# Kernel optimization log

Measured on AMD Instinct MI355X. Metric: run time of the kernel, lower is better.

The kernel has to match this reference:

```python
import jax, jax.numpy as jnp
import numpy as np

B, N, D_IN, D_HID, D_EDGE = 4, 256, 256, 256, 64


def setup_inputs() -> dict:
    key = jax.random.key(0)
    ks = jax.random.split(key, 8)
    s_in = 1.0 / np.sqrt(D_IN)
    s_h2 = 1.0 / np.sqrt(2 * D_HID)
    s_h = 1.0 / np.sqrt(D_HID)
    return {
        "x": jax.random.normal(ks[0], (B, N, D_IN), jnp.float32),
        "W_in": jax.random.uniform(ks[1], (D_HID, D_IN), jnp.float32, -s_in, s_in),
        "b_in": jax.random.uniform(ks[2], (D_HID,), jnp.float32, -s_in, s_in),
        "W1": jax.random.uniform(ks[3], (D_HID, 2 * D_HID), jnp.float32, -s_h2, s_h2),
        "b1": jax.random.uniform(ks[4], (D_HID,), jnp.float32, -s_h2, s_h2),
        "W2": jax.random.uniform(ks[5], (D_EDGE, D_HID), jnp.float32, -s_h, s_h),
        "b2": jax.random.uniform(ks[6], (D_EDGE,), jnp.float32, -s_h, s_h),
    }


def reference(x, W_in, b_in, W1, b1, W2, b2):
    # in_proj: [B,N,d_in] -> [B,N,h]
    h = jnp.einsum("bnd,hd->bnh", x, W_in) + b_in
    # cat([h_i, h_j]) @ W1 == h_i @ Wa + h_j @ Wb with W1 = [Wa | Wb].
    # Precompute the two N x h projections, then broadcast-add over the pair grid
    # instead of materializing the [B,N,N,2h] concat (same math, fused form).
    Wa, Wb = W1[:, :D_HID], W1[:, D_HID:]
    pa = jnp.einsum("bnh,gh->bng", h, Wa)  # [B,N,h]
    pb = jnp.einsum("bnh,gh->bng", h, Wb)  # [B,N,h]
    z = pa[:, :, None, :] + pb[:, None, :, :] + b1  # [B,N,N,h]
    z = z * jax.nn.sigmoid(z)  # Swish
    return jnp.einsum("bijh,eh->bije", z, W2) + b2  # [B,N,N,d_edge]
```

## Files before the change

kernel.cpp:

```cpp
#include <hip/hip_runtime.h>

#define DIN 256
#define DHID 256
#define DEDGE 64
#define GS 68
#define W2_PAD 264

typedef float f32x4 __attribute__((ext_vector_type(4)));
typedef short s16x8 __attribute__((ext_vector_type(8)));
typedef unsigned int u32x4 __attribute__((ext_vector_type(4)));

__device__ __forceinline__ unsigned short f2bf(float f) {
    unsigned int u = __builtin_bit_cast(unsigned int, f);
    u += 0x7fffu + ((u >> 16) & 1u);
    return (unsigned short)(u >> 16);
}
__device__ __forceinline__ unsigned int pk_bf16(float a, float b) {
    return (unsigned int)f2bf(a) | ((unsigned int)f2bf(b) << 16);
}

__global__ __launch_bounds__(256) void k_xh(
    const float* __restrict__ x, const float* __restrict__ Win,
    float* __restrict__ hp)
{
    __shared__ float as[64 * GS];
    __shared__ float ws[64 * GS];
    const int m0 = blockIdx.x << 6, n0 = blockIdx.y << 6, k0 = blockIdx.z << 6;
    const int tid = threadIdx.x;
    const int rr = tid >> 4;
    const int kk = (tid & 15) << 2;

#pragma unroll
    for (int it = 0; it < 4; ++it) {
        const int row = rr + (it << 4);
        *reinterpret_cast<f32x4*>(&as[row * GS + kk]) =
            *reinterpret_cast<const f32x4*>(&x[(m0 + row) * DIN + k0 + kk]);
        *reinterpret_cast<f32x4*>(&ws[row * GS + kk]) =
            *reinterpret_cast<const f32x4*>(&Win[(n0 + row) * DIN + k0 + kk]);
    }
    __syncthreads();

    const int tx = tid & 15, ty = tid >> 4;
    float acc[4][4] = {};
    for (int k = 0; k < 64; k += 4) {
        f32x4 av[4], wv[4];
#pragma unroll
        for (int r = 0; r < 4; ++r)
            av[r] = *reinterpret_cast<const f32x4*>(&as[(ty + (r << 4)) * GS + k]);
#pragma unroll
        for (int c = 0; c < 4; ++c)
            wv[c] = *reinterpret_cast<const f32x4*>(&ws[(tx + (c << 4)) * GS + k]);
#pragma unroll
        for (int r = 0; r < 4; ++r)
#pragma unroll
            for (int c = 0; c < 4; ++c)
                acc[r][c] += av[r][0]*wv[c][0] + av[r][1]*wv[c][1]
                           + av[r][2]*wv[c][2] + av[r][3]*wv[c][3];
    }
    float* dst = hp + ((size_t)blockIdx.z << 18);
#pragma unroll
    for (int r = 0; r < 4; ++r)
#pragma unroll
        for (int c = 0; c < 4; ++c)
            dst[(m0 + ty + (r << 4)) * DHID + n0 + tx + (c << 4)] = acc[r][c];
}

__global__ __launch_bounds__(256) void k_pab(
    const float* __restrict__ hp, const float* __restrict__ W1,
    const float* __restrict__ bin, float* __restrict__ pap, float* __restrict__ pbp)
{
    __shared__ float as[64 * GS];
    __shared__ float ws[64 * GS];
    const int m0 = blockIdx.x << 6;
    const int half = blockIdx.y >> 2;
    const int n0 = (blockIdx.y & 3) << 6;
    const int kc = blockIdx.z;
    const int tid = threadIdx.x;
    const int rr = tid >> 4, kk = (tid & 15) << 2;
    const int tx = tid & 15, ty = tid >> 4;

    float acc[4][4] = {};
    for (int kt = 0; kt < 2; ++kt) {
        const int k0 = (kc << 7) + (kt << 6);
        if (kt) __syncthreads();
#pragma unroll
        for (int it = 0; it < 4; ++it) {
            const int row = rr + (it << 4);
            const int aoff = (m0 + row) * DHID + k0 + kk;
            f32x4 av = *reinterpret_cast<const f32x4*>(&hp[aoff]);
            av += *reinterpret_cast<const f32x4*>(&hp[aoff + (1 << 18)]);
            av += *reinterpret_cast<const f32x4*>(&hp[aoff + (2 << 18)]);
            av += *reinterpret_cast<const f32x4*>(&hp[aoff + (3 << 18)]);
            av += *reinterpret_cast<const f32x4*>(&bin[k0 + kk]);
            *reinterpret_cast<f32x4*>(&as[row * GS + kk]) = av;
            *reinterpret_cast<f32x4*>(&ws[row * GS + kk]) =
                *reinterpret_cast<const f32x4*>(&W1[(n0 + row) * 512 + (half << 8) + k0 + kk]);
        }
        __syncthreads();

        for (int k = 0; k < 64; k += 4) {
            f32x4 av[4], wv[4];
#pragma unroll
            for (int r = 0; r < 4; ++r)
                av[r] = *reinterpret_cast<const f32x4*>(&as[(ty + (r << 4)) * GS + k]);
#pragma unroll
            for (int c = 0; c < 4; ++c)
                wv[c] = *reinterpret_cast<const f32x4*>(&ws[(tx + (c << 4)) * GS + k]);
#pragma unroll
            for (int r = 0; r < 4; ++r)
#pragma unroll
                for (int c = 0; c < 4; ++c)
                    acc[r][c] += av[r][0]*wv[c][0] + av[r][1]*wv[c][1]
                               + av[r][2]*wv[c][2] + av[r][3]*wv[c][3];
        }
    }
    float* dst = (half ? pbp : pap) + ((size_t)kc << 18);
#pragma unroll
    for (int r = 0; r < 4; ++r)
#pragma unroll
        for (int c = 0; c < 4; ++c)
            dst[(m0 + ty + (r << 4)) * DHID + n0 + tx + (c << 4)] = acc[r][c];
}

__global__ __launch_bounds__(256) void k_out(
    const float* __restrict__ pap, const float* __restrict__ pbp,
    const float* __restrict__ b1, const float* __restrict__ W2,
    const float* __restrict__ b2, float* __restrict__ out)
{
    __shared__ unsigned short w2s[DEDGE * W2_PAD];
    __shared__ float pab1[4][DHID];

    const int jb = blockIdx.x, i0 = blockIdx.y << 2, b = blockIdx.z;
    const int tid = threadIdx.x;

    {
        const float b1v = b1[tid];
#pragma unroll
        for (int ii = 0; ii < 4; ++ii) {
            const int off = (((b << 8) + i0 + ii) << 8) + tid;
            pab1[ii][tid] = pap[off] + pap[off + (1 << 18)] + b1v;
        }
    }
#pragma unroll
    for (int it = 0; it < 8; ++it) {
        const int t = tid + (it << 8);
        const int row = t >> 5;
        const int cc = (t & 31) << 3;
        const f32x4 w0 = *reinterpret_cast<const f32x4*>(&W2[row * DHID + cc]);
        const f32x4 w1 = *reinterpret_cast<const f32x4*>(&W2[row * DHID + cc + 4]);
        u32x4 wp;
        wp[0] = pk_bf16(w0[0], w0[1]); wp[1] = pk_bf16(w0[2], w0[3]);
        wp[2] = pk_bf16(w1[0], w1[1]); wp[3] = pk_bf16(w1[2], w1[3]);
        *reinterpret_cast<u32x4*>(&w2s[row * W2_PAD + cc]) = wp;
    }
    __syncthreads();

    const int lane = tid & 63, wave = tid >> 6, quad = lane >> 4, l15 = lane & 15;
    const int j0 = (jb << 6) + (wave << 4);
    const int pboff = (((b << 8) + (j0 + l15)) << 8);
    const float* pbq0 = pbp + pboff;
    const float* pbq1 = pbp + (1 << 18) + pboff;

    f32x4 acc[4][4];
#pragma unroll
    for (int ii = 0; ii < 4; ++ii)
#pragma unroll
        for (int eb = 0; eb < 4; ++eb) acc[ii][eb] = (f32x4){0.f, 0.f, 0.f, 0.f};

    float b2v[4];
#pragma unroll
    for (int eb = 0; eb < 4; ++eb) b2v[eb] = b2[(eb << 4) + l15];

    for (int k0 = 0; k0 < 8; ++k0) {
        const int g = (k0 << 5) + (quad << 3);
        const f32x4 p0 = *reinterpret_cast<const f32x4*>(pbq0 + g)
                       + *reinterpret_cast<const f32x4*>(pbq1 + g);
        const f32x4 p1 = *reinterpret_cast<const f32x4*>(pbq0 + g + 4)
                       + *reinterpret_cast<const f32x4*>(pbq1 + g + 4);

        s16x8 bfrag[4];
#pragma unroll
        for (int eb = 0; eb < 4; ++eb)
            bfrag[eb] = *reinterpret_cast<const s16x8*>(&w2s[((eb << 4) + l15) * W2_PAD + g]);

#pragma unroll
        for (int ii = 0; ii < 4; ++ii) {
            const f32x4 q0 = *reinterpret_cast<const f32x4*>(&pab1[ii][g]);
            const f32x4 q1 = *reinterpret_cast<const f32x4*>(&pab1[ii][g + 4]);
            float s[8];
#pragma unroll
            for (int jj = 0; jj < 4; ++jj) {
                const float z0 = q0[jj] + p0[jj];
                const float z1 = q1[jj] + p1[jj];
                const float e0 = __expf(-z0);
                const float e1 = __expf(-z1);
                s[jj]     = z0 * __builtin_amdgcn_rcpf(1.0f + e0);
                s[4 + jj] = z1 * __builtin_amdgcn_rcpf(1.0f + e1);
            }
            u32x4 ap;
            ap[0] = pk_bf16(s[0], s[1]); ap[1] = pk_bf16(s[2], s[3]);
            ap[2] = pk_bf16(s[4], s[5]); ap[3] = pk_bf16(s[6], s[7]);
            const s16x8 a = __builtin_bit_cast(s16x8, ap);
#pragma unroll
            for (int eb = 0; eb < 4; ++eb)
                acc[ii][eb] = __builtin_amdgcn_mfma_f32_16x16x32_bf16(a, bfrag[eb], acc[ii][eb], 0, 0, 0);
        }
    }

#pragma unroll
    for (int ii = 0; ii < 4; ++ii) {
        const int obase = (((((b << 8) + i0 + ii) << 8) + j0 + (quad << 2)) << 6) + l15;
#pragma unroll
        for (int eb = 0; eb < 4; ++eb) {
#pragma unroll
            for (int r = 0; r < 4; ++r)
                out[obase + (r << 6) + (eb << 4)] = acc[ii][eb][r] + b2v[eb];
        }
    }
}

extern "C" void kernel_launch(void* const* d_in, const int* in_sizes, int n_in,
                              void* d_out, int out_size, void* d_ws, size_t ws_size,
                              hipStream_t stream) {
    const float* x = 0; const float* Win = 0; const float* bin = 0;
    const float* W1 = 0; const float* b1 = 0; const float* W2 = 0; const float* b2 = 0;
    for (int idx = 0; idx < n_in; ++idx) {
        const int s = in_sizes[idx];
        if (s == 262144) x = (const float*)d_in[idx];
        else if (s == 131072) W1 = (const float*)d_in[idx];
        else if (s == 65536) Win = (const float*)d_in[idx];
        else if (s == 16384) W2 = (const float*)d_in[idx];
        else if (s == 64) b2 = (const float*)d_in[idx];
        else if (s == 256) { if (!bin) bin = (const float*)d_in[idx]; else b1 = (const float*)d_in[idx]; }
    }

    float* ws = (float*)d_ws;
    float* hp  = ws;
    float* pap = hp + (4 << 18);
    float* pbp = pap + (2 << 18);

    hipLaunchKernelGGL(k_xh,  dim3(16, 4, 4), dim3(256), 0, stream, x, Win, hp);
    hipLaunchKernelGGL(k_pab, dim3(16, 8, 2), dim3(256), 0, stream, hp, W1, bin, pap, pbp);
    hipLaunchKernelGGL(k_out, dim3(4, 64, 4), dim3(256), 0, stream, pap, pbp, b1, W2, b2, (float*)d_out);
}
```

Before: 130.3 us.

## Fold in_proj into W1, pre-swizzle W2 in LDS, use hardware bf16 packing

Folds the input projection into the first layer by precomputing W1a·Win and W1b·Win plus a combined bias in a small weight-only kernel, so the activation path applies x directly to the combined weights instead of materializing h. W2 is stored in LDS already laid out in MFMA fragment order, so each lane reads its fragment with one indexed load. The software bf16 rounding is replaced with the v_cvt_pk_bf16_f32 instruction, and the large output is written with nontemporal stores. These target the k_out epilogue and conversion overhead and the cost of the first kernel, at the price of a different summation order in the folded weights.

```diff
diff --git a/kernel.cpp b/kernel.cpp
--- a/kernel.cpp
+++ b/kernel.cpp
@@ -4,73 +4,94 @@
 #define DHID 256
 #define DEDGE 64
 #define GS 68
-#define W2_PAD 264
 
 typedef float f32x4 __attribute__((ext_vector_type(4)));
 typedef short s16x8 __attribute__((ext_vector_type(8)));
 typedef unsigned int u32x4 __attribute__((ext_vector_type(4)));
 
-__device__ __forceinline__ unsigned short f2bf(float f) {
-    unsigned int u = __builtin_bit_cast(unsigned int, f);
-    u += 0x7fffu + ((u >> 16) & 1u);
-    return (unsigned short)(u >> 16);
-}
-__device__ __forceinline__ unsigned int pk_bf16(float a, float b) {
-    return (unsigned int)f2bf(a) | ((unsigned int)f2bf(b) << 16);
-}
-
-__global__ __launch_bounds__(256) void k_xh(
-    const float* __restrict__ x, const float* __restrict__ Win,
-    float* __restrict__ hp)
+__device__ __forceinline__ unsigned int cvtpk(float lo, float hi) {
+    unsigned int r;
+    asm("v_cvt_pk_bf16_f32 %0, %1, %2" : "=v"(r) : "v"(lo), "v"(hi));
+    return r;
+}
+
+__global__ __launch_bounds__(256) void k_w(
+    const float* __restrict__ Win, const float* __restrict__ W1,
+    const float* __restrict__ bin, const float* __restrict__ b1,
+    float* __restrict__ CWp, float* __restrict__ cb)
+{
+    const int bid = blockIdx.x;
+    const int tid = threadIdx.x;
+    if (bid == 64) {
+        float acc = b1[tid];
+        const float* wrow = &W1[tid * 512];
+        for (int h = 0; h < 256; h += 4) {
+            const f32x4 wa = *reinterpret_cast<const f32x4*>(&wrow[h]);
+            const f32x4 wb = *reinterpret_cast<const f32x4*>(&wrow[256 + h]);
+            const f32x4 bv = *reinterpret_cast<const f32x4*>(&bin[h]);
+            acc += (wa[0]+wb[0])*bv[0] + (wa[1]+wb[1])*bv[1]
+                 + (wa[2]+wb[2])*bv[2] + (wa[3]+wb[3])*bv[3];
+        }
+        cb[tid] = acc;
+        return;
+    }
+    __shared__ float as[64 * GS];
+    __shared__ float ws2[64 * GS];
+    const int kc = bid >> 5;
+    const int nt = (bid >> 2) & 7;
+    const int dt = bid & 3;
+    const int n0 = nt << 6, d0 = dt << 6;
+    const int na = n0 & 255;
+    const int hb = (n0 >> 8) << 8;
+    const int rr = tid >> 4, kk = (tid & 15) << 2;
+    const int tx = tid & 15, ty = tid >> 4;
+
+    float acc[4][4] = {};
+    for (int kt = 0; kt < 2; ++kt) {
+        const int h0 = (kc << 7) + (kt << 6);
+        if (kt) __syncthreads();
+#pragma unroll
+        for (int it = 0; it < 4; ++it) {
+            const int row = rr + (it << 4);
+            *reinterpret_cast<f32x4*>(&as[row * GS + kk]) =
+                *reinterpret_cast<const f32x4*>(&W1[(na + row) * 512 + hb + h0 + kk]);
+            *reinterpret_cast<f32x4*>(&ws2[row * GS + kk]) =
+                *reinterpret_cast<const f32x4*>(&Win[(h0 + row) * DIN + d0 + kk]);
+        }
+        __syncthreads();
+        for (int k = 0; k < 64; k += 4) {
+            f32x4 av[4];
+#pragma unroll
+            for (int r = 0; r < 4; ++r)
+                av[r] = *reinterpret_cast<const f32x4*>(&as[(ty + (r << 4)) * GS + k]);
+#pragma unroll
+            for (int k2 = 0; k2 < 4; ++k2) {
+                float bcol[4];
+#pragma unroll
+                for (int c = 0; c < 4; ++c)
+                    bcol[c] = ws2[(k + k2) * GS + tx + (c << 4)];
+#pragma unroll
+                for (int r = 0; r < 4; ++r)
+#pragma unroll
+                    for (int c = 0; c < 4; ++c)
+                        acc[r][c] += av[r][k2] * bcol[c];
+            }
+        }
+    }
+    float* dst = CWp + ((size_t)kc << 17);
+#pragma unroll
+    for (int r = 0; r < 4; ++r)
+#pragma unroll
+        for (int c = 0; c < 4; ++c)
+            dst[(n0 + ty + (r << 4)) * 256 + d0 + tx + (c << 4)] = acc[r][c];
+}
+
+__global__ __launch_bounds__(256) void k_pab(
+    const float* __restrict__ x, const float* __restrict__ CWp,
+    float* __restrict__ pap, float* __restrict__ pbp)
 {
     __shared__ float as[64 * GS];
-    __shared__ float ws[64 * GS];
-    const int m0 = blockIdx.x << 6, n0 = blockIdx.y << 6, k0 = blockIdx.z << 6;
-    const int tid = threadIdx.x;
-    const int rr = tid >> 4;
-    const int kk = (tid & 15) << 2;
-
-#pragma unroll
-    for (int it = 0; it < 4; ++it) {
-        const int row = rr + (it << 4);
-        *reinterpret_cast<f32x4*>(&as[row * GS + kk]) =
-            *reinterpret_cast<const f32x4*>(&x[(m0 + row) * DIN + k0 + kk]);
-        *reinterpret_cast<f32x4*>(&ws[row * GS + kk]) =
-            *reinterpret_cast<const f32x4*>(&Win[(n0 + row) * DIN + k0 + kk]);
-    }
-    __syncthreads();
-
-    const int tx = tid & 15, ty = tid >> 4;
-    float acc[4][4] = {};
-    for (int k = 0; k < 64; k += 4) {
-        f32x4 av[4], wv[4];
-#pragma unroll
-        for (int r = 0; r < 4; ++r)
-            av[r] = *reinterpret_cast<const f32x4*>(&as[(ty + (r << 4)) * GS + k]);
-#pragma unroll
-        for (int c = 0; c < 4; ++c)
-            wv[c] = *reinterpret_cast<const f32x4*>(&ws[(tx + (c << 4)) * GS + k]);
-#pragma unroll
-        for (int r = 0; r < 4; ++r)
-#pragma unroll
-            for (int c = 0; c < 4; ++c)
-                acc[r][c] += av[r][0]*wv[c][0] + av[r][1]*wv[c][1]
-                           + av[r][2]*wv[c][2] + av[r][3]*wv[c][3];
-    }
-    float* dst = hp + ((size_t)blockIdx.z << 18);
-#pragma unroll
-    for (int r = 0; r < 4; ++r)
-#pragma unroll
-        for (int c = 0; c < 4; ++c)
-            dst[(m0 + ty + (r << 4)) * DHID + n0 + tx + (c << 4)] = acc[r][c];
-}
-
-__global__ __launch_bounds__(256) void k_pab(
-    const float* __restrict__ hp, const float* __restrict__ W1,
-    const float* __restrict__ bin, float* __restrict__ pap, float* __restrict__ pbp)
-{
-    __shared__ float as[64 * GS];
-    __shared__ float ws[64 * GS];
+    __shared__ float ws2[64 * GS];
     const int m0 = blockIdx.x << 6;
     const int half = blockIdx.y >> 2;
     const int n0 = (blockIdx.y & 3) << 6;
@@ -86,15 +107,12 @@
 #pragma unroll
         for (int it = 0; it < 4; ++it) {
             const int row = rr + (it << 4);
-            const int aoff = (m0 + row) * DHID + k0 + kk;
-            f32x4 av = *reinterpret_cast<const f32x4*>(&hp[aoff]);
-            av += *reinterpret_cast<const f32x4*>(&hp[aoff + (1 << 18)]);
-            av += *reinterpret_cast<const f32x4*>(&hp[aoff + (2 << 18)]);
-            av += *reinterpret_cast<const f32x4*>(&hp[aoff + (3 << 18)]);
-            av += *reinterpret_cast<const f32x4*>(&bin[k0 + kk]);
-            *reinterpret_cast<f32x4*>(&as[row * GS + kk]) = av;
-            *reinterpret_cast<f32x4*>(&ws[row * GS + kk]) =
-                *reinterpret_cast<const f32x4*>(&W1[(n0 + row) * 512 + (half << 8) + k0 + kk]);
+            *reinterpret_cast<f32x4*>(&as[row * GS + kk]) =
+                *reinterpret_cast<const f32x4*>(&x[(m0 + row) * DIN + k0 + kk]);
+            const float* wr = &CWp[((half << 8) + n0 + row) * 256 + k0 + kk];
+            const f32x4 wv = *reinterpret_cast<const f32x4*>(wr)
+                           + *reinterpret_cast<const f32x4*>(wr + (1 << 17));
+            *reinterpret_cast<f32x4*>(&ws2[row * GS + kk]) = wv;
         }
         __syncthreads();
 
@@ -105,7 +123,7 @@
                 av[r] = *reinterpret_cast<const f32x4*>(&as[(ty + (r << 4)) * GS + k]);
 #pragma unroll
             for (int c = 0; c < 4; ++c)
-                wv[c] = *reinterpret_cast<const f32x4*>(&ws[(tx + (c << 4)) * GS + k]);
+                wv[c] = *reinterpret_cast<const f32x4*>(&ws2[(tx + (c << 4)) * GS + k]);
 #pragma unroll
             for (int r = 0; r < 4; ++r)
 #pragma unroll
@@ -124,34 +142,35 @@
 
 __global__ __launch_bounds__(256) void k_out(
     const float* __restrict__ pap, const float* __restrict__ pbp,
-    const float* __restrict__ b1, const float* __restrict__ W2,
+    const float* __restrict__ cb, const float* __restrict__ W2,
     const float* __restrict__ b2, float* __restrict__ out)
 {
-    __shared__ unsigned short w2s[DEDGE * W2_PAD];
+    __shared__ s16x8 w2s[2048];
     __shared__ float pab1[4][DHID];
 
     const int jb = blockIdx.x, i0 = blockIdx.y << 2, b = blockIdx.z;
     const int tid = threadIdx.x;
 
     {
-        const float b1v = b1[tid];
+        const float cv = cb[tid];
 #pragma unroll
         for (int ii = 0; ii < 4; ++ii) {
             const int off = (((b << 8) + i0 + ii) << 8) + tid;
-            pab1[ii][tid] = pap[off] + pap[off + (1 << 18)] + b1v;
+            pab1[ii][tid] = pap[off] + pap[off + (1 << 18)] + cv;
         }
     }
 #pragma unroll
     for (int it = 0; it < 8; ++it) {
-        const int t = tid + (it << 8);
-        const int row = t >> 5;
-        const int cc = (t & 31) << 3;
-        const f32x4 w0 = *reinterpret_cast<const f32x4*>(&W2[row * DHID + cc]);
-        const f32x4 w1 = *reinterpret_cast<const f32x4*>(&W2[row * DHID + cc + 4]);
+        const int f = tid + (it << 8);
+        const int l15f = f & 15, qf = (f >> 4) & 3, ebf = (f >> 6) & 3, k0f = f >> 8;
+        const int row = (ebf << 4) + l15f;
+        const int col = (k0f << 5) + (qf << 3);
+        const f32x4 w0 = *reinterpret_cast<const f32x4*>(&W2[row * DHID + col]);
+        const f32x4 w1 = *reinterpret_cast<const f32x4*>(&W2[row * DHID + col + 4]);
         u32x4 wp;
-        wp[0] = pk_bf16(w0[0], w0[1]); wp[1] = pk_bf16(w0[2], w0[3]);
-        wp[2] = pk_bf16(w1[0], w1[1]); wp[3] = pk_bf16(w1[2], w1[3]);
-        *reinterpret_cast<u32x4*>(&w2s[row * W2_PAD + cc]) = wp;
+        wp[0] = cvtpk(w0[0], w0[1]); wp[1] = cvtpk(w0[2], w0[3]);
+        wp[2] = cvtpk(w1[0], w1[1]); wp[3] = cvtpk(w1[2], w1[3]);
+        w2s[f] = __builtin_bit_cast(s16x8, wp);
     }
     __syncthreads();
 
@@ -181,7 +200,7 @@
         s16x8 bfrag[4];
 #pragma unroll
         for (int eb = 0; eb < 4; ++eb)
-            bfrag[eb] = *reinterpret_cast<const s16x8*>(&w2s[((eb << 4) + l15) * W2_PAD + g]);
+            bfrag[eb] = w2s[((k0 << 2) + eb) * 64 + lane];
 
 #pragma unroll
         for (int ii = 0; ii < 4; ++ii) {
@@ -198,8 +217,8 @@
                 s[4 + jj] = z1 * __builtin_amdgcn_rcpf(1.0f + e1);
             }
             u32x4 ap;
-            ap[0] = pk_bf16(s[0], s[1]); ap[1] = pk_bf16(s[2], s[3]);
-            ap[2] = pk_bf16(s[4], s[5]); ap[3] = pk_bf16(s[6], s[7]);
+            ap[0] = cvtpk(s[0], s[1]); ap[1] = cvtpk(s[2], s[3]);
+            ap[2] = cvtpk(s[4], s[5]); ap[3] = cvtpk(s[6], s[7]);
             const s16x8 a = __builtin_bit_cast(s16x8, ap);
 #pragma unroll
             for (int eb = 0; eb < 4; ++eb)
@@ -214,7 +233,8 @@
         for (int eb = 0; eb < 4; ++eb) {
 #pragma unroll
             for (int r = 0; r < 4; ++r)
-                out[obase + (r << 6) + (eb << 4)] = acc[ii][eb][r] + b2v[eb];
+                __builtin_nontemporal_store(acc[ii][eb][r] + b2v[eb],
+                                            &out[obase + (r << 6) + (eb << 4)]);
         }
     }
 }
@@ -235,11 +255,12 @@
     }
 
     float* ws = (float*)d_ws;
-    float* hp  = ws;
-    float* pap = hp + (4 << 18);
-    float* pbp = pap + (2 << 18);
-
-    hipLaunchKernelGGL(k_xh,  dim3(16, 4, 4), dim3(256), 0, stream, x, Win, hp);
-    hipLaunchKernelGGL(k_pab, dim3(16, 8, 2), dim3(256), 0, stream, hp, W1, bin, pap, pbp);
-    hipLaunchKernelGGL(k_out, dim3(4, 64, 4), dim3(256), 0, stream, pap, pbp, b1, W2, b2, (float*)d_out);
-}
+    float* CWp = ws;
+    float* cb  = ws + (1 << 18);
+    float* pap = ws + (1 << 18) + 256;
+    float* pbp = pap + (1 << 19);
+
+    hipLaunchKernelGGL(k_w,   dim3(65),       dim3(256), 0, stream, Win, W1, bin, b1, CWp, cb);
+    hipLaunchKernelGGL(k_pab, dim3(16, 8, 2), dim3(256), 0, stream, x, CWp, pap, pbp);
+    hipLaunchKernelGGL(k_out, dim3(4, 64, 4), dim3(256), 0, stream, pap, pbp, cb, W2, b2, (float*)d_out);
+}
```

After: 145.7 us. +11.8%, slower.
